# Optimization experiments

Measured on AMD Instinct MI355X. Metric: run time of the kernel, lower is better.

## Reference

```python
import jax, jax.numpy as jnp
import numpy as np


def setup_inputs() -> dict:
    key = jax.random.key(0)
    k1, k2, k3, k4, k5 = jax.random.split(key, 5)
    T, R, K, D = 8, 512, 4, 4096          # tiles, rows/tile, group size, in_features
    N_CW = 16384                           # codebook size
    N_TOK = 512                            # tokens
    x = jax.random.normal(k1, (N_TOK, D), dtype=jnp.float32)
    codewords = jax.random.normal(k2, (N_CW, D), dtype=jnp.float32) * 0.02
    indices = jax.random.randint(k3, (T, R, K), 0, N_CW, dtype=jnp.int64)
    rotations = jax.random.normal(k4, (T, D, D), dtype=jnp.float32) * (1.0 / np.sqrt(D))
    scales = jax.random.uniform(k5, (T,), dtype=jnp.float32) + 0.5
    bias = jnp.zeros((D,), dtype=jnp.float32)
    return {"x": x, "codewords": codewords, "indices": indices,
            "rotations": rotations, "scales": scales, "bias": bias}


def reference(x, codewords, indices, rotations, scales, bias):
    # Decode weight tiles: gather [T,R,K,D] -> mean over group -> [T,R,D]
    decoded = codewords[indices].mean(axis=2)
    # Per-tile rotation and scale: [T,R,D] @ [T,D,D] -> [T,R,D]
    decoded = jnp.einsum('trd,tde->tre', decoded, rotations) * scales[:, None, None]
    T, R, D = decoded.shape
    weight = decoded.reshape(T * R, D)     # [out_features, in_features]
    # Linear: x @ W^T + b
    return x @ weight.T + bias
```

## Files before the change

### kernel.cpp

```cpp
#include <hip/hip_runtime.h>

typedef unsigned int uint32;
typedef unsigned short u16;
typedef float fx4 __attribute__((ext_vector_type(4)));
typedef uint32 u32x4 __attribute__((ext_vector_type(4)));

typedef const __attribute__((address_space(1))) void gvoid;
typedef __attribute__((address_space(3))) void lvoid;

#define MFMA_BF16_16x16x32(acc, a, b) \
  asm("v_mfma_f32_16x16x32_bf16 %0, %1, %2, %0" : "+v"(acc) : "v"(a), "v"(b))

#define WAIT_LGKM0() asm volatile("s_waitcnt lgkmcnt(0)" ::: "memory")
#define WAIT_VM0()   asm volatile("s_waitcnt vmcnt(0)" ::: "memory")
#define WAIT_VM3()   asm volatile("s_waitcnt vmcnt(3)" ::: "memory")
#define WAIT_VM4()   asm volatile("s_waitcnt vmcnt(4)" ::: "memory")
#define WAIT_VM6()   asm volatile("s_waitcnt vmcnt(6)" ::: "memory")
#define WAIT_VM8()   asm volatile("s_waitcnt vmcnt(8)" ::: "memory")
#define WAIT_VM10()  asm volatile("s_waitcnt vmcnt(10)" ::: "memory")
#define SFENCE()     __builtin_amdgcn_sched_barrier(0)
#define BARRIER()    do { __builtin_amdgcn_s_barrier(); asm volatile("" ::: "memory"); } while (0)
#define NOWAIT()     do { } while (0)

__device__ __forceinline__ u16 f2bf_rne(float f) {
  uint32 u = __builtin_bit_cast(uint32, f);
  u += 0x7FFFu + ((u >> 16) & 1u);
  return (u16)(u >> 16);
}

__device__ __forceinline__ uint32 cvt_pk_bf16(float lo, float hi) {
  uint32 r;
  asm("v_cvt_pk_bf16_f32 %0, %1, %2" : "=v"(r) : "v"(lo), "v"(hi));
  return r;
}

__global__ __launch_bounds__(256) void cvtx_kernel(const float* __restrict__ x,
                                                   u16* __restrict__ xb) {
  const int i = blockIdx.x * 256 + threadIdx.x;
  float4 v = ((const float4*)x)[i];
  ushort4 o;
  o.x = f2bf_rne(v.x);
  o.y = f2bf_rne(v.y);
  o.z = f2bf_rne(v.z);
  o.w = f2bf_rne(v.w);
  ((ushort4*)xb)[i] = o;
}

__global__ __launch_bounds__(256) void decode_kernel(
    const float* __restrict__ cw, const int* __restrict__ indices,
    const float* __restrict__ scales, u16* __restrict__ dec) {
  const int row = blockIdx.x;
  const int t = row >> 9;
  const int* ip = indices + (size_t)row * 4;
  const float* c0 = cw + (size_t)ip[0] * 4096;
  const float* c1 = cw + (size_t)ip[1] * 4096;
  const float* c2 = cw + (size_t)ip[2] * 4096;
  const float* c3 = cw + (size_t)ip[3] * 4096;
  const float s = scales[t] * 0.25f;
  u16* orow = dec + (size_t)row * 4096;
  const int tid = threadIdx.x;
#pragma unroll
  for (int j = 0; j < 4; ++j) {
    const int d = j * 1024 + tid * 4;
    float4 a = *(const float4*)(c0 + d);
    float4 b = *(const float4*)(c1 + d);
    float4 c = *(const float4*)(c2 + d);
    float4 e = *(const float4*)(c3 + d);
    ushort4 o;
    o.x = f2bf_rne((a.x + b.x + c.x + e.x) * s);
    o.y = f2bf_rne((a.y + b.y + c.y + e.y) * s);
    o.z = f2bf_rne((a.z + b.z + c.z + e.z) * s);
    o.w = f2bf_rne((a.w + b.w + c.w + e.w) * s);
    *(ushort4*)(orow + d) = o;
  }
}

__global__ __launch_bounds__(512, 2) void gemm_z_kernel(
    const u16* __restrict__ Xb,
    const float* __restrict__ rot,
    u16* __restrict__ Z) {
  __shared__ char sA[65536];
  __shared__ char sB[65536];

  const int lb = blockIdx.x;
  const int swz = ((lb & 7) << 5) | (lb >> 3);
  const int t = swz >> 5;
  const int rem = swz & 31;
  const int nb = rem >> 1, mb = rem & 1;
  const float* Bt = rot + ((size_t)t << 24);
  u16* Ct = Z + ((size_t)t << 21);
  const int aRow0 = mb << 8, bCol0 = nb << 8;
  const int tid = threadIdx.x;
  const int wv = tid >> 6, ln = tid & 63;
  const int lr = ln & 15, lk = ln >> 4;
  const int wr = wv >> 2, wc = wv & 3;

  fx4 acc[8][4] = {};

  const u16* Asrc = Xb + (size_t)(aRow0 + (tid >> 3)) * 4096 +
                    (((tid & 7) ^ ((tid >> 3) & 7)) << 3);
  const float* Bsrc = Bt + (size_t)(bCol0 + (tid >> 3)) * 4096 + ((tid & 7) << 3);
  const int bwr = (tid >> 3) * 128 + (((tid & 7) ^ ((tid >> 3) & 7)) << 4);
  const int cs0 = (lk ^ (lr & 7)) << 4;
  const int cs1 = ((4 + lk) ^ (lr & 7)) << 4;
  const int aB = (wr * 128 + lr) * 128;
  const int bB = (wc * 64 + lr) * 128;

#define STAGE_A4(DB, KT)                                                      \
  _Pragma("unroll")                                                           \
  for (int c = 0; c < 4; ++c)                                                 \
    __builtin_amdgcn_global_load_lds(                                         \
        (gvoid*)(Asrc + (size_t)(c << 6) * 4096 + ((KT) << 6)),               \
        (lvoid*)(sA + (DB) * 32768 + (c << 13) + (wv << 10) + ln * 16),       \
        16, 0, 0)

#define LOADB_S(KT, SL)                                                       \
  do {                                                                        \
    const float* bp_ = Bsrc + (size_t)((SL) << 6) * 4096 + ((KT) << 6);       \
    S[2 * (SL)] = *(const float4*)(bp_);                                      \
    S[2 * (SL) + 1] = *(const float4*)(bp_ + 4);                              \
  } while (0)

#define PACK_S(DSTB, SL)                                                      \
  do {                                                                        \
    u32x4 w_;                                                                 \
    w_[0] = cvt_pk_bf16(S[2 * (SL)].x, S[2 * (SL)].y);                        \
    w_[1] = cvt_pk_bf16(S[2 * (SL)].z, S[2 * (SL)].w);                        \
    w_[2] = cvt_pk_bf16(S[2 * (SL) + 1].x, S[2 * (SL) + 1].y);                \
    w_[3] = cvt_pk_bf16(S[2 * (SL) + 1].z, S[2 * (SL) + 1].w);                \
    *(u32x4*)((DSTB) + ((SL) << 13) + bwr) = w_;                              \
  } while (0)

#define READS_A(D, MH)                                                        \
  do {                                                                        \
    const char* pA_ = sA + (D) * 32768 + ((MH) << 13) + aB;                   \
    af[0][0] = *(const u32x4*)(pA_ + cs0);                                    \
    af[0][1] = *(const u32x4*)(pA_ + cs1);                                    \
    af[1][0] = *(const u32x4*)(pA_ + 2048 + cs0);                             \
    af[1][1] = *(const u32x4*)(pA_ + 2048 + cs1);                             \
    af[2][0] = *(const u32x4*)(pA_ + 4096 + cs0);                             \
    af[2][1] = *(const u32x4*)(pA_ + 4096 + cs1);                             \
    af[3][0] = *(const u32x4*)(pA_ + 6144 + cs0);                             \
    af[3][1] = *(const u32x4*)(pA_ + 6144 + cs1);                             \
  } while (0)
#define READS_B(D, NH)                                                        \
  do {                                                                        \
    const char* pB_ = sB + (D) * 32768 + ((NH) << 12) + bB;                   \
    bf[0][0] = *(const u32x4*)(pB_ + cs0);                                    \
    bf[0][1] = *(const u32x4*)(pB_ + cs1);                                    \
    bf[1][0] = *(const u32x4*)(pB_ + 2048 + cs0);                             \
    bf[1][1] = *(const u32x4*)(pB_ + 2048 + cs1);                             \
  } while (0)

#define MFMA_Q(MH, NH)                                                        \
  do {                                                                        \
    __builtin_amdgcn_s_setprio(1);                                            \
    _Pragma("unroll")                                                         \
    for (int m = 0; m < 4; ++m)                                               \
      _Pragma("unroll")                                                       \
      for (int n = 0; n < 2; ++n) {                                           \
        MFMA_BF16_16x16x32(acc[(MH) * 4 + m][(NH) * 2 + n], af[m][0],         \
                           bf[n][0]);                                         \
        MFMA_BF16_16x16x32(acc[(MH) * 4 + m][(NH) * 2 + n], af[m][1],         \
                           bf[n][1]);                                         \
      }                                                                       \
    __builtin_amdgcn_s_setprio(0);                                            \
  } while (0)

#define ITER_Z(D, KT, DOPACK, DOSTAGE, DOLOAD, HV0, HV1, HV2, HV3, TV)        \
  do {                                                                        \
              \
    HV0;                                                                      \
    SFENCE();                                                                 \
    if (DOPACK) { PACK_S(sB + ((D) ^ 1) * 32768, 0); }                        \
    SFENCE();                                                                 \
    READS_A(D, 0);                                                            \
    READS_B(D, 0);                                                            \
    SFENCE();                                                                 \
    if (DOSTAGE) { STAGE_A4((D) ^ 1, (KT) + 1); }                             \
    SFENCE();                                                                 \
    if (DOLOAD) { LOADB_S((KT) + 2, 0); }                                     \
    SFENCE();                                                                 \
    BARRIER();                                                                \
    WAIT_LGKM0();                                                             \
    SFENCE();                                                                 \
    MFMA_Q(0, 0);                                                             \
    BARRIER();                                                                \
                                     \
    HV1;                                                                      \
    SFENCE();                                                                 \
    if (DOPACK) { PACK_S(sB + ((D) ^ 1) * 32768, 1); }                        \
    SFENCE();                                                                 \
    READS_A(D, 1);                                                            \
    SFENCE();                                                                 \
    if (DOLOAD) { LOADB_S((KT) + 2, 1); }                                     \
    SFENCE();                                                                 \
    BARRIER();                                                                \
    WAIT_LGKM0();                                                             \
    SFENCE();                                                                 \
    MFMA_Q(1, 0);                                                             \
    BARRIER();                                                                \
                                     \
    HV2;                                                                      \
    SFENCE();                                                                 \
    if (DOPACK) { PACK_S(sB + ((D) ^ 1) * 32768, 2); }                        \
    SFENCE();                                                                 \
    READS_B(D, 1);                                                            \
    SFENCE();                                                                 \
    if (DOLOAD) { LOADB_S((KT) + 2, 2); }                                     \
    SFENCE();                                                                 \
    BARRIER();                                                                \
    WAIT_LGKM0();                                                             \
    SFENCE();                                                                 \
    MFMA_Q(1, 1);                                                             \
    BARRIER();                                                                \
                               \
    HV3;                                                                      \
    SFENCE();                                                                 \
    if (DOPACK) { PACK_S(sB + ((D) ^ 1) * 32768, 3); }                        \
    SFENCE();                                                                 \
    READS_A(D, 0);                                                            \
    SFENCE();                                                                 \
    if (DOLOAD) { LOADB_S((KT) + 2, 3); }                                     \
    SFENCE();                                                                 \
    BARRIER();                                                                \
    WAIT_LGKM0();                                                             \
    SFENCE();                                                                 \
    MFMA_Q(0, 1);                                                             \
    TV;                                                                       \
    BARRIER();                                                                \
  } while (0)

  u32x4 af[4][2], bf[2][2];
  float4 S[8];

  STAGE_A4(0, 0);
  SFENCE();
  LOADB_S(0, 0); LOADB_S(0, 1); LOADB_S(0, 2); LOADB_S(0, 3);
  SFENCE();
  WAIT_VM0();
  SFENCE();
  PACK_S(sB, 0); PACK_S(sB, 1); PACK_S(sB, 2); PACK_S(sB, 3);
  SFENCE();
  LOADB_S(1, 0); LOADB_S(1, 1); LOADB_S(1, 2); LOADB_S(1, 3);
  SFENCE();
  WAIT_LGKM0();
  BARRIER();

#pragma unroll 1
  for (int kt = 0; kt < 62; ++kt) {
    const int d = kt & 1;
    ITER_Z(d, kt, 1, 1, 1, WAIT_VM6(), WAIT_VM10(), WAIT_VM10(), WAIT_VM10(),
           WAIT_VM8());
  }
  ITER_Z(0, 62, 1, 1, 0, WAIT_VM6(), WAIT_VM8(), WAIT_VM6(), WAIT_VM4(),
         WAIT_VM0());
  ITER_Z(1, 63, 0, 0, 0, NOWAIT(), NOWAIT(), NOWAIT(), NOWAIT(), NOWAIT());

#pragma unroll
  for (int m = 0; m < 8; ++m) {
    const int r0 = aRow0 + wr * 128 + m * 16 + lk * 4;
#pragma unroll
    for (int n = 0; n < 4; ++n) {
      const int col = bCol0 + wc * 64 + n * 16 + lr;
#pragma unroll
      for (int j = 0; j < 4; ++j)
        Ct[(size_t)(r0 + j) * 4096 + col] = f2bf_rne(acc[m][n][j]);
    }
  }
#undef STAGE_A4
#undef LOADB_S
#undef PACK_S
#undef READS_A
#undef READS_B
#undef MFMA_Q
#undef ITER_Z
}

__global__ __launch_bounds__(256, 2) void gemm_out_kernel(
    const u16* __restrict__ Z,
    const u16* __restrict__ Dec,
    float* __restrict__ part) {
  __shared__ char sm[49152];
  const int lb = blockIdx.x;
  const int sp = lb >> 8;
  const int ls = lb & 255;
  const int swz = ((ls & 7) << 5) | (ls >> 3);
  const int t = swz >> 5;
  const int rem = swz & 31;
  const int nb = rem >> 2, mb = rem & 3;
  const u16* At = Z + ((size_t)t << 21);
  const u16* Bt = Dec + ((size_t)t << 21);
  float* po = part + (size_t)sp * (512 * 4096);
  const int aRow0 = mb << 7, bCol0 = nb << 6;
  const int KS = sp << 11;
  const int tid = threadIdx.x;
  const int wv = tid >> 6, ln = tid & 63;
  const int lr = ln & 15, lk = ln >> 4;
  const int wr = wv >> 1, wc = wv & 1;

  fx4 acc[4][2] = {};

  const int kswz = (((tid & 3) ^ ((tid >> 3) & 3)) << 3);
  const u16* Asrc = At + (size_t)(aRow0 + (tid >> 2)) * 4096 + KS + kswz;
  const u16* Bsrc = Bt + (size_t)(bCol0 + (tid >> 2)) * 4096 + KS + kswz;
  const int gr = (lr >> 1) & 3;
  const int aof = (wr * 64 + lr) * 64 + ((lk ^ gr) << 4);
  const int bof = 8192 + (wc * 32 + lr) * 64 + ((lk ^ gr) << 4);

#define STAGE_O(buf, kofs)                                                   \
  do {                                                                       \
    _Pragma("unroll")                                                        \
    for (int c = 0; c < 2; ++c)                                              \
      __builtin_amdgcn_global_load_lds(                                      \
          (gvoid*)(Asrc + (size_t)(c << 6) * 4096 + (kofs)),                 \
          (lvoid*)((buf) + c * 4096 + tid * 16), 16, 0, 0);                  \
    __builtin_amdgcn_global_load_lds((gvoid*)(Bsrc + (kofs)),                \
                                     (lvoid*)((buf) + 8192 + tid * 16), 16,  \
                                     0, 0);                                  \
  } while (0)

  char* b0 = sm;
  char* b1 = sm + 12288;
  char* b2 = sm + 24576;
  char* b3 = sm + 36864;
  STAGE_O(b0, 0);
  STAGE_O(b1, 32);
  STAGE_O(b2, 64);
  WAIT_VM6();
  BARRIER();

#pragma unroll 1
  for (int kt = 0; kt < 64; ++kt) {
    if (kt + 3 < 64) STAGE_O(b3, (kt + 3) << 5);
    u32x4 af[4], bf[2];
#pragma unroll
    for (int m = 0; m < 4; ++m)
      af[m] = *(const u32x4*)(b0 + aof + m * 1024);
#pragma unroll
    for (int n = 0; n < 2; ++n)
      bf[n] = *(const u32x4*)(b0 + bof + n * 1024);
    WAIT_LGKM0();
    SFENCE();
#pragma unroll
    for (int m = 0; m < 4; ++m)
#pragma unroll
      for (int n = 0; n < 2; ++n)
        MFMA_BF16_16x16x32(acc[m][n], af[m], bf[n]);
    if (kt + 3 < 64) {
      WAIT_VM6();
    } else if (kt + 2 < 64) {
      WAIT_VM3();
    } else {
      WAIT_VM0();
    }
    BARRIER();
    char* tmp = b0; b0 = b1; b1 = b2; b2 = b3; b3 = tmp;
  }

#pragma unroll
  for (int n = 0; n < 2; ++n) {
    const int colg = (t << 9) + bCol0 + wc * 32 + n * 16 + lr;
#pragma unroll
    for (int m = 0; m < 4; ++m) {
      const int r0 = aRow0 + wr * 64 + m * 16 + lk * 4;
#pragma unroll
      for (int j = 0; j < 4; ++j)
        po[(size_t)(r0 + j) * 4096 + colg] = acc[m][n][j];
    }
  }
#undef STAGE_O
}

__global__ __launch_bounds__(256) void combine_kernel(
    const float* __restrict__ p0, const float* __restrict__ p1,
    const float* __restrict__ bias, float* __restrict__ out) {
  const int i = blockIdx.x * 256 + threadIdx.x;
  float4 a = ((const float4*)p0)[i];
  float4 b = ((const float4*)p1)[i];
  float4 bv = ((const float4*)bias)[i & 1023];
  float4 o;
  o.x = a.x + b.x + bv.x;
  o.y = a.y + b.y + bv.y;
  o.z = a.z + b.z + bv.z;
  o.w = a.w + b.w + bv.w;
  ((float4*)out)[i] = o;
}

extern "C" void kernel_launch(void* const* d_in, const int* in_sizes, int n_in,
                              void* d_out, int out_size, void* d_ws, size_t ws_size,
                              hipStream_t stream) {
  const float* x       = (const float*)d_in[0];
  const float* cw      = (const float*)d_in[1];
  const int*   indices = (const int*)d_in[2];
  const float* rot     = (const float*)d_in[3];
  const float* scales  = (const float*)d_in[4];
  const float* bias    = (const float*)d_in[5];
  float* out = (float*)d_out;
  char* ws = (char*)d_ws;

  u16*   xb   = (u16*)(ws);
  u16*   dec  = (u16*)(ws + ((size_t)4 << 20));
  u16*   z    = (u16*)(ws + ((size_t)36 << 20));
  float* part = (float*)(ws + ((size_t)68 << 20));

  decode_kernel<<<dim3(4096), dim3(256), 0, stream>>>(cw, indices, scales, dec);
  cvtx_kernel<<<dim3(2048), dim3(256), 0, stream>>>(x, xb);
  gemm_z_kernel<<<dim3(256), dim3(512), 0, stream>>>(xb, rot, z);
  gemm_out_kernel<<<dim3(512), dim3(256), 0, stream>>>(z, dec, part);
  combine_kernel<<<dim3(2048), dim3(256), 0, stream>>>(
      part, part + (size_t)512 * 4096, bias, out);
}
```

Before: 279.4 us.

## Fuse decode into Z GEMM launch and drop split-K with combine kernel

The codebook decode now runs on 256 extra blocks inside the Z GEMM launch, 16 rows per block, so it overlaps with the GEMM blocks instead of being a separate kernel. The output GEMM no longer splits K in two halves. It runs the full 128 K-steps per block and adds the bias directly in its epilogue, so the partial buffers and the combine kernel are gone. The costs are that the output GEMM now launches only 256 blocks, which lowers parallelism on a chip with 256 CUs. The decode blocks also reserve the fused kernel's 128 KB of LDS and may compete with the GEMM blocks for CU slots.

Measured after the change: 278.2 us. About the same (-0.4%).

```diff
diff --git a/kernel.cpp b/kernel.cpp
--- a/kernel.cpp
+++ b/kernel.cpp
@@ -46,43 +46,53 @@
   ((ushort4*)xb)[i] = o;
 }
 
-__global__ __launch_bounds__(256) void decode_kernel(
+__device__ __forceinline__ void decode_body(
+    int bid, const float* __restrict__ cw, const int* __restrict__ indices,
+    const float* __restrict__ scales, u16* __restrict__ dec) {
+  const int tid = threadIdx.x;
+#pragma unroll 1
+  for (int rr = 0; rr < 16; ++rr) {
+    const int row = bid * 16 + rr;
+    const int t = row >> 9;
+    const int* ip = indices + (size_t)row * 4;
+    const float* c0 = cw + (size_t)ip[0] * 4096;
+    const float* c1 = cw + (size_t)ip[1] * 4096;
+    const float* c2 = cw + (size_t)ip[2] * 4096;
+    const float* c3 = cw + (size_t)ip[3] * 4096;
+    const float s = scales[t] * 0.25f;
+    u16* orow = dec + (size_t)row * 4096;
+#pragma unroll
+    for (int j = 0; j < 2; ++j) {
+      const int d = j * 2048 + tid * 4;
+      float4 a = *(const float4*)(c0 + d);
+      float4 b = *(const float4*)(c1 + d);
+      float4 c = *(const float4*)(c2 + d);
+      float4 e = *(const float4*)(c3 + d);
+      ushort4 o;
+      o.x = f2bf_rne((a.x + b.x + c.x + e.x) * s);
+      o.y = f2bf_rne((a.y + b.y + c.y + e.y) * s);
+      o.z = f2bf_rne((a.z + b.z + c.z + e.z) * s);
+      o.w = f2bf_rne((a.w + b.w + c.w + e.w) * s);
+      *(ushort4*)(orow + d) = o;
+    }
+  }
+}
+
+__global__ __launch_bounds__(512, 2) void fused_z_decode_kernel(
+    const u16* __restrict__ Xb,
+    const float* __restrict__ rot,
+    u16* __restrict__ Z,
     const float* __restrict__ cw, const int* __restrict__ indices,
     const float* __restrict__ scales, u16* __restrict__ dec) {
-  const int row = blockIdx.x;
-  const int t = row >> 9;
-  const int* ip = indices + (size_t)row * 4;
-  const float* c0 = cw + (size_t)ip[0] * 4096;
-  const float* c1 = cw + (size_t)ip[1] * 4096;
-  const float* c2 = cw + (size_t)ip[2] * 4096;
-  const float* c3 = cw + (size_t)ip[3] * 4096;
-  const float s = scales[t] * 0.25f;
-  u16* orow = dec + (size_t)row * 4096;
-  const int tid = threadIdx.x;
-#pragma unroll
-  for (int j = 0; j < 4; ++j) {
-    const int d = j * 1024 + tid * 4;
-    float4 a = *(const float4*)(c0 + d);
-    float4 b = *(const float4*)(c1 + d);
-    float4 c = *(const float4*)(c2 + d);
-    float4 e = *(const float4*)(c3 + d);
-    ushort4 o;
-    o.x = f2bf_rne((a.x + b.x + c.x + e.x) * s);
-    o.y = f2bf_rne((a.y + b.y + c.y + e.y) * s);
-    o.z = f2bf_rne((a.z + b.z + c.z + e.z) * s);
-    o.w = f2bf_rne((a.w + b.w + c.w + e.w) * s);
-    *(ushort4*)(orow + d) = o;
-  }
-}
-
-__global__ __launch_bounds__(512, 2) void gemm_z_kernel(
-    const u16* __restrict__ Xb,
-    const float* __restrict__ rot,
-    u16* __restrict__ Z) {
   __shared__ char sA[65536];
   __shared__ char sB[65536];
 
-  const int lb = blockIdx.x;
+  const int bid = blockIdx.x;
+  if (bid < 256) {
+    decode_body(bid, cw, indices, scales, dec);
+    return;
+  }
+  const int lb = bid - 256;
   const int swz = ((lb & 7) << 5) | (lb >> 3);
   const int t = swz >> 5;
   const int rem = swz & 31;
@@ -169,7 +179,6 @@
 
 #define ITER_Z(D, KT, DOPACK, DOSTAGE, DOLOAD, HV0, HV1, HV2, HV3, TV)        \
   do {                                                                        \
-              \
     HV0;                                                                      \
     SFENCE();                                                                 \
     if (DOPACK) { PACK_S(sB + ((D) ^ 1) * 32768, 0); }                        \
@@ -186,7 +195,6 @@
     SFENCE();                                                                 \
     MFMA_Q(0, 0);                                                             \
     BARRIER();                                                                \
-                                     \
     HV1;                                                                      \
     SFENCE();                                                                 \
     if (DOPACK) { PACK_S(sB + ((D) ^ 1) * 32768, 1); }                        \
@@ -200,7 +208,6 @@
     SFENCE();                                                                 \
     MFMA_Q(1, 0);                                                             \
     BARRIER();                                                                \
-                                     \
     HV2;                                                                      \
     SFENCE();                                                                 \
     if (DOPACK) { PACK_S(sB + ((D) ^ 1) * 32768, 2); }                        \
@@ -214,7 +221,6 @@
     SFENCE();                                                                 \
     MFMA_Q(1, 1);                                                             \
     BARRIER();                                                                \
-                               \
     HV3;                                                                      \
     SFENCE();                                                                 \
     if (DOPACK) { PACK_S(sB + ((D) ^ 1) * 32768, 3); }                        \
@@ -280,20 +286,17 @@
 __global__ __launch_bounds__(256, 2) void gemm_out_kernel(
     const u16* __restrict__ Z,
     const u16* __restrict__ Dec,
-    float* __restrict__ part) {
+    const float* __restrict__ bias,
+    float* __restrict__ out) {
   __shared__ char sm[49152];
   const int lb = blockIdx.x;
-  const int sp = lb >> 8;
-  const int ls = lb & 255;
-  const int swz = ((ls & 7) << 5) | (ls >> 3);
+  const int swz = ((lb & 7) << 5) | (lb >> 3);
   const int t = swz >> 5;
   const int rem = swz & 31;
   const int nb = rem >> 2, mb = rem & 3;
   const u16* At = Z + ((size_t)t << 21);
   const u16* Bt = Dec + ((size_t)t << 21);
-  float* po = part + (size_t)sp * (512 * 4096);
   const int aRow0 = mb << 7, bCol0 = nb << 6;
-  const int KS = sp << 11;
   const int tid = threadIdx.x;
   const int wv = tid >> 6, ln = tid & 63;
   const int lr = ln & 15, lk = ln >> 4;
@@ -302,8 +305,8 @@
   fx4 acc[4][2] = {};
 
   const int kswz = (((tid & 3) ^ ((tid >> 3) & 3)) << 3);
-  const u16* Asrc = At + (size_t)(aRow0 + (tid >> 2)) * 4096 + KS + kswz;
-  const u16* Bsrc = Bt + (size_t)(bCol0 + (tid >> 2)) * 4096 + KS + kswz;
+  const u16* Asrc = At + (size_t)(aRow0 + (tid >> 2)) * 4096 + kswz;
+  const u16* Bsrc = Bt + (size_t)(bCol0 + (tid >> 2)) * 4096 + kswz;
   const int gr = (lr >> 1) & 3;
   const int aof = (wr * 64 + lr) * 64 + ((lk ^ gr) << 4);
   const int bof = 8192 + (wc * 32 + lr) * 64 + ((lk ^ gr) << 4);
@@ -331,8 +334,8 @@
   BARRIER();
 
 #pragma unroll 1
-  for (int kt = 0; kt < 64; ++kt) {
-    if (kt + 3 < 64) STAGE_O(b3, (kt + 3) << 5);
+  for (int kt = 0; kt < 128; ++kt) {
+    if (kt + 3 < 128) STAGE_O(b3, (kt + 3) << 5);
     u32x4 af[4], bf[2];
 #pragma unroll
     for (int m = 0; m < 4; ++m)
@@ -347,9 +350,9 @@
 #pragma unroll
       for (int n = 0; n < 2; ++n)
         MFMA_BF16_16x16x32(acc[m][n], af[m], bf[n]);
-    if (kt + 3 < 64) {
+    if (kt + 3 < 128) {
       WAIT_VM6();
-    } else if (kt + 2 < 64) {
+    } else if (kt + 2 < 128) {
       WAIT_VM3();
     } else {
       WAIT_VM0();
@@ -361,30 +364,16 @@
 #pragma unroll
   for (int n = 0; n < 2; ++n) {
     const int colg = (t << 9) + bCol0 + wc * 32 + n * 16 + lr;
+    const float bv = bias[colg];
 #pragma unroll
     for (int m = 0; m < 4; ++m) {
       const int r0 = aRow0 + wr * 64 + m * 16 + lk * 4;
 #pragma unroll
       for (int j = 0; j < 4; ++j)
-        po[(size_t)(r0 + j) * 4096 + colg] = acc[m][n][j];
+        out[(size_t)(r0 + j) * 4096 + colg] = acc[m][n][j] + bv;
     }
   }
 #undef STAGE_O
-}
-
-__global__ __launch_bounds__(256) void combine_kernel(
-    const float* __restrict__ p0, const float* __restrict__ p1,
-    const float* __restrict__ bias, float* __restrict__ out) {
-  const int i = blockIdx.x * 256 + threadIdx.x;
-  float4 a = ((const float4*)p0)[i];
-  float4 b = ((const float4*)p1)[i];
-  float4 bv = ((const float4*)bias)[i & 1023];
-  float4 o;
-  o.x = a.x + b.x + bv.x;
-  o.y = a.y + b.y + bv.y;
-  o.z = a.z + b.z + bv.z;
-  o.w = a.w + b.w + bv.w;
-  ((float4*)out)[i] = o;
 }
 
 extern "C" void kernel_launch(void* const* d_in, const int* in_sizes, int n_in,
@@ -399,15 +388,12 @@
   float* out = (float*)d_out;
   char* ws = (char*)d_ws;
 
-  u16*   xb   = (u16*)(ws);
-  u16*   dec  = (u16*)(ws + ((size_t)4 << 20));
-  u16*   z    = (u16*)(ws + ((size_t)36 << 20));
-  float* part = (float*)(ws + ((size_t)68 << 20));
-
-  decode_kernel<<<dim3(4096), dim3(256), 0, stream>>>(cw, indices, scales, dec);
+  u16* xb  = (u16*)(ws);
+  u16* dec = (u16*)(ws + ((size_t)4 << 20));
+  u16* z   = (u16*)(ws + ((size_t)36 << 20));
+
   cvtx_kernel<<<dim3(2048), dim3(256), 0, stream>>>(x, xb);
-  gemm_z_kernel<<<dim3(256), dim3(512), 0, stream>>>(xb, rot, z);
-  gemm_out_kernel<<<dim3(512), dim3(256), 0, stream>>>(z, dec, part);
-  combine_kernel<<<dim3(2048), dim3(256), 0, stream>>>(
-      part, part + (size_t)512 * 4096, bias, out);
-}
+  fused_z_decode_kernel<<<dim3(512), dim3(512), 0, stream>>>(
+      xb, rot, z, cw, indices, scales, dec);
+  gemm_out_kernel<<<dim3(256), dim3(256), 0, stream>>>(z, dec, bias, out);
+}
```
